# Performance work log

Measured on AMD Instinct MI355X. Metric: run time of the kernel, lower is better.

Reference implementation:

```python
import jax, jax.numpy as jnp
import numpy as np

DIM = 1024
B, SQ, SK = 8, 2048, 2048


def setup_inputs() -> dict:
    key = jax.random.key(0)
    ks = jax.random.split(key, 8)
    s = 1.0 / np.sqrt(DIM)
    return {
        "x": jax.random.normal(ks[0], (B, SQ, DIM), dtype=jnp.float32),
        "context": jax.random.normal(ks[1], (B, SK, DIM), dtype=jnp.float32),
        "Wq": jax.random.normal(ks[2], (DIM, DIM), dtype=jnp.float32) * s,
        "bq": jnp.zeros((DIM,), dtype=jnp.float32),
        "Wk": jax.random.normal(ks[3], (DIM, DIM), dtype=jnp.float32) * s,
        "bk": jnp.zeros((DIM,), dtype=jnp.float32),
        "Wv": jax.random.normal(ks[4], (DIM, DIM), dtype=jnp.float32) * s,
        "bv": jnp.zeros((DIM,), dtype=jnp.float32),
    }


def reference(x, context, Wq, bq, Wk, bk, Wv, bv):
    # nn.Linear: y = x @ W.T + b
    q = jnp.einsum("bsd,ed->bse", x, Wq) + bq          # [B, SQ, D]
    k = jnp.einsum("btd,ed->bte", context, Wk) + bk    # [B, SK, D]
    v = jnp.einsum("btd,ed->bte", context, Wv) + bv    # [B, SK, D]
    scale = 1.0 / jnp.sqrt(jnp.asarray(x.shape[-1], dtype=x.dtype))
    scores = jnp.einsum("bse,bte->bst", q, k) * scale  # [B, SQ, SK]
    attn = jax.nn.softmax(scores, axis=-1)
    return jnp.einsum("bst,bte->bse", attn, v)         # [B, SQ, D]
```

## Files before the change

kernel.cpp:

```cpp
#include <hip/hip_runtime.h>
#include <hip/hip_bf16.h>
#include <hip/hip_fp16.h>

typedef float f32x4 __attribute__((ext_vector_type(4)));
typedef short short8 __attribute__((ext_vector_type(8)));
typedef _Float16 h4 __attribute__((ext_vector_type(4)));
typedef unsigned short u16;
typedef unsigned int u32;

#define LDK 40

__device__ __forceinline__ u16 bf16_rne(float x) {
  u32 u = __float_as_uint(x);
  u += 0x7FFFu + ((u >> 16) & 1u);
  return (u16)(u >> 16);
}
__device__ __forceinline__ u32 pack2(float a, float b) {
  return (u32)bf16_rne(a) | ((u32)bf16_rne(b) << 16);
}

__global__ __launch_bounds__(256)
void convert_kernel(const float* __restrict__ x, const float* __restrict__ ctx,
                    const float* __restrict__ wq, const float* __restrict__ wk,
                    const float* __restrict__ wv,
                    u16* __restrict__ xb, u16* __restrict__ cb,
                    u16* __restrict__ wqb, u16* __restrict__ wkb,
                    u16* __restrict__ wvb)
{
  int blk = blockIdx.x;
  const float* src; u16* dst; size_t off;
  if (blk < 8192)       { src = x;   dst = xb;  off = (size_t)blk * 2048; }
  else if (blk < 16384) { src = ctx; dst = cb;  off = (size_t)(blk - 8192) * 2048; }
  else if (blk < 16896) { src = wq;  dst = wqb; off = (size_t)(blk - 16384) * 2048; }
  else if (blk < 17408) { src = wk;  dst = wkb; off = (size_t)(blk - 16896) * 2048; }
  else                  { src = wv;  dst = wvb; off = (size_t)(blk - 17408) * 2048; }
  size_t e = off + (size_t)threadIdx.x * 8;
  float4 a = *(const float4*)(src + e);
  float4 b = *(const float4*)(src + e + 4);
  uint4 o;
  o.x = pack2(a.x, a.y); o.y = pack2(a.z, a.w);
  o.z = pack2(b.x, b.y); o.w = pack2(b.z, b.w);
  *(uint4*)(dst + e) = o;
}

__device__ __forceinline__ void stage_tile(const u16* __restrict__ G, int ld,
                                           int kt, u16* L, int tid) {
#pragma unroll
  for (int it = 0; it < 2; ++it) {
    int s = tid + 256 * it;
    int r = s >> 2, c = s & 3;
    *(uint4*)&L[r * LDK + c * 8] = *(const uint4*)(G + (size_t)r * ld + kt + c * 8);
  }
}

#define GEMM_FRAGS_AND_MFMA(Ah, Bh)                                            \
  short8 a_f[4], b_f[4];                                                       \
  _Pragma("unroll")                                                            \
  for (int i = 0; i < 4; ++i) {                                                \
    a_f[i] = *(const short8*)&Ah[(wm + i * 16 + lrow) * LDK + quad * 8];       \
    b_f[i] = *(const short8*)&Bh[(wn + i * 16 + lrow) * LDK + quad * 8];       \
  }                                                                            \
  _Pragma("unroll")                                                            \
  for (int i = 0; i < 4; ++i)                                                  \
    _Pragma("unroll")                                                          \
    for (int j = 0; j < 4; ++j)                                                \
      acc[i][j] = __builtin_amdgcn_mfma_f32_16x16x32_bf16(a_f[i], b_f[j], acc[i][j], 0, 0, 0);

#define GEMM_PROLOGUE                                                          \
  const int tid = threadIdx.x;                                                 \
  const int w = tid >> 6, lane = tid & 63;                                     \
  const int wm = (w >> 1) * 64, wn = (w & 1) * 64;                             \
  const int lrow = lane & 15, quad = lane >> 4;                                \
  f32x4 acc[4][4];                                                             \
  _Pragma("unroll")                                                            \
  for (int i = 0; i < 4; ++i)                                                  \
    _Pragma("unroll")                                                          \
    for (int j = 0; j < 4; ++j) {                                              \
      f32x4 z = {0.f, 0.f, 0.f, 0.f};                                          \
      acc[i][j] = z;                                                           \
    }

__global__ __launch_bounds__(256)
void projq_kernel(const u16* __restrict__ A, const u16* __restrict__ W,
                  const float* __restrict__ bias, u16* __restrict__ Y)
{
  __shared__ __align__(16) u16 Ah[128 * LDK];
  __shared__ __align__(16) u16 Bh[128 * LDK];
  const int m0 = blockIdx.y * 128, n0 = blockIdx.x * 128;
  GEMM_PROLOGUE
  const u16* A_b = A + (size_t)m0 * 1024;
  const u16* B_b = W + (size_t)n0 * 1024;

  for (int kt = 0; kt < 1024; kt += 32) {
    __syncthreads();
    stage_tile(A_b, 1024, kt, Ah, tid);
    stage_tile(B_b, 1024, kt, Bh, tid);
    __syncthreads();
    GEMM_FRAGS_AND_MFMA(Ah, Bh)
  }

#pragma unroll
  for (int j = 0; j < 4; ++j) {
    int gn = n0 + wn + j * 16 + lrow;
    float bj = bias[gn];
#pragma unroll
    for (int i = 0; i < 4; ++i) {
      int gm_base = m0 + wm + i * 16 + quad * 4;
#pragma unroll
      for (int r = 0; r < 4; ++r)
        Y[(size_t)(gm_base + r) * 1024 + gn] = bf16_rne(acc[i][j][r] + bj);
    }
  }
}

__global__ __launch_bounds__(256)
void projv_kernel(const u16* __restrict__ A, const u16* __restrict__ W,
                  const float* __restrict__ bias, u16* __restrict__ Vt)
{
  __shared__ __align__(16) u16 smem[128 * 136];
  u16* Ah = smem;
  u16* Bh = smem + 128 * LDK;
  const int m0 = blockIdx.y * 128, n0 = blockIdx.x * 128;
  const int bb = m0 >> 11, t0 = m0 & 2047;
  GEMM_PROLOGUE
  const u16* A_b = A + (size_t)m0 * 1024;
  const u16* B_b = W + (size_t)n0 * 1024;

  for (int kt = 0; kt < 1024; kt += 32) {
    __syncthreads();
    stage_tile(A_b, 1024, kt, Ah, tid);
    stage_tile(B_b, 1024, kt, Bh, tid);
    __syncthreads();
    GEMM_FRAGS_AND_MFMA(Ah, Bh)
  }

  __syncthreads();
  u16* T = smem;
#pragma unroll
  for (int j = 0; j < 4; ++j) {
    int e_l = wn + j * 16 + lrow;
    float bj = bias[n0 + e_l];
#pragma unroll
    for (int i = 0; i < 4; ++i) {
      int t_l = wm + i * 16 + quad * 4;
      uint2 p;
      p.x = pack2(acc[i][j][0] + bj, acc[i][j][1] + bj);
      p.y = pack2(acc[i][j][2] + bj, acc[i][j][3] + bj);
      *(uint2*)&T[e_l * 136 + t_l] = p;
    }
  }
  __syncthreads();

  int e_l = tid >> 1, half = tid & 1;
  u16* gdst = Vt + ((size_t)(bb * 1024 + n0 + e_l)) * 2048 + t0 + half * 64;
  const u16* Trow = &T[e_l * 136 + half * 64];
#pragma unroll
  for (int k = 0; k < 8; ++k)
    *(uint4*)(gdst + k * 8) = *(const uint4*)(Trow + k * 8);
}

__global__ __launch_bounds__(256)
void score_kernel(const u16* __restrict__ qb, const u16* __restrict__ kb,
                  _Float16* __restrict__ S)
{
  __shared__ __align__(16) u16 Ah[128 * LDK];
  __shared__ __align__(16) u16 Bh[128 * LDK];
  const int b = blockIdx.z;
  const int m0 = blockIdx.y * 128, n0 = blockIdx.x * 128;
  GEMM_PROLOGUE
  const u16* A_b = qb + ((size_t)b * 2048 + m0) * 1024;
  const u16* B_b = kb + ((size_t)b * 2048 + n0) * 1024;

  for (int kt = 0; kt < 1024; kt += 32) {
    __syncthreads();
    stage_tile(A_b, 1024, kt, Ah, tid);
    stage_tile(B_b, 1024, kt, Bh, tid);
    __syncthreads();
    GEMM_FRAGS_AND_MFMA(Ah, Bh)
  }

  const float scale = 0.03125f;
#pragma unroll
  for (int j = 0; j < 4; ++j) {
    int gn = n0 + wn + j * 16 + lrow;
#pragma unroll
    for (int i = 0; i < 4; ++i) {
      int gm_base = m0 + wm + i * 16 + quad * 4;
#pragma unroll
      for (int r = 0; r < 4; ++r)
        S[((size_t)b * 2048 + gm_base + r) * 2048 + gn] = (_Float16)(acc[i][j][r] * scale);
    }
  }
}

__global__ __launch_bounds__(256)
void softmax_kernel(_Float16* __restrict__ S)
{
  const int row = blockIdx.x;
  const int tid = threadIdx.x;
  _Float16* Sr = S + (size_t)row * 2048;
  h4 ah = *(const h4*)(Sr + tid * 4);
  h4 bh = *(const h4*)(Sr + 1024 + tid * 4);
  float a0 = (float)ah.x, a1 = (float)ah.y, a2 = (float)ah.z, a3 = (float)ah.w;
  float b0 = (float)bh.x, b1 = (float)bh.y, b2 = (float)bh.z, b3 = (float)bh.w;

  float m = fmaxf(fmaxf(fmaxf(a0, a1), fmaxf(a2, a3)),
                  fmaxf(fmaxf(b0, b1), fmaxf(b2, b3)));
#pragma unroll
  for (int off = 32; off > 0; off >>= 1) m = fmaxf(m, __shfl_xor(m, off));

  __shared__ float red[4];
  const int wid = tid >> 6, lane = tid & 63;
  if (lane == 0) red[wid] = m;
  __syncthreads();
  m = fmaxf(fmaxf(red[0], red[1]), fmaxf(red[2], red[3]));

  float e0 = __expf(a0 - m), e1 = __expf(a1 - m), e2 = __expf(a2 - m), e3 = __expf(a3 - m);
  float e4 = __expf(b0 - m), e5 = __expf(b1 - m), e6 = __expf(b2 - m), e7 = __expf(b3 - m);
  float s = ((e0 + e1) + (e2 + e3)) + ((e4 + e5) + (e6 + e7));
#pragma unroll
  for (int off = 32; off > 0; off >>= 1) s += __shfl_xor(s, off);
  __syncthreads();
  if (lane == 0) red[wid] = s;
  __syncthreads();
  s = red[0] + red[1] + red[2] + red[3];
  float inv = 1.0f / s;

  u16* P = (u16*)S;
  size_t pb = (size_t)row * 2048;
  uint2 w0, w1;
  w0.x = pack2(e0 * inv, e1 * inv);
  w0.y = pack2(e2 * inv, e3 * inv);
  w1.x = pack2(e4 * inv, e5 * inv);
  w1.y = pack2(e6 * inv, e7 * inv);
  *(uint2*)&P[pb + tid * 4] = w0;
  *(uint2*)&P[pb + 1024 + tid * 4] = w1;
}

__global__ __launch_bounds__(256)
void pv_kernel(const u16* __restrict__ P, const u16* __restrict__ Vt,
               float* __restrict__ O)
{
  __shared__ __align__(16) u16 Ah[128 * LDK];
  __shared__ __align__(16) u16 Bh[128 * LDK];
  const int b = blockIdx.z;
  const int m0 = blockIdx.y * 128, n0 = blockIdx.x * 128;
  GEMM_PROLOGUE
  const u16* A_b = P + ((size_t)b * 2048 + m0) * 2048;
  const u16* B_b = Vt + ((size_t)b * 1024 + n0) * 2048;

  for (int kt = 0; kt < 2048; kt += 32) {
    __syncthreads();
    stage_tile(A_b, 2048, kt, Ah, tid);
    stage_tile(B_b, 2048, kt, Bh, tid);
    __syncthreads();
    GEMM_FRAGS_AND_MFMA(Ah, Bh)
  }

#pragma unroll
  for (int j = 0; j < 4; ++j) {
    int gn = n0 + wn + j * 16 + lrow;
#pragma unroll
    for (int i = 0; i < 4; ++i) {
      int gm_base = m0 + wm + i * 16 + quad * 4;
#pragma unroll
      for (int r = 0; r < 4; ++r)
        O[((size_t)b * 2048 + gm_base + r) * 1024 + gn] = acc[i][j][r];
    }
  }
}

extern "C" void kernel_launch(void* const* d_in, const int* in_sizes, int n_in,
                              void* d_out, int out_size, void* d_ws, size_t ws_size,
                              hipStream_t stream) {
  const float* x   = (const float*)d_in[0];
  const float* ctx = (const float*)d_in[1];
  const float* Wq  = (const float*)d_in[2];
  const float* bq  = (const float*)d_in[3];
  const float* Wk  = (const float*)d_in[4];
  const float* bk  = (const float*)d_in[5];
  const float* Wv  = (const float*)d_in[6];
  const float* bv  = (const float*)d_in[7];
  float* out = (float*)d_out;

  const size_t NQ = (size_t)16384 * 1024;
  const size_t NW = (size_t)1024 * 1024;
  const size_t needed = (5 * NQ + 3 * NW) * sizeof(u16);
  if (ws_size < needed) return;

  u16* xb  = (u16*)d_ws;
  u16* cb  = xb + NQ;
  u16* qb  = cb + NQ;
  u16* kb  = qb + NQ;
  u16* vt  = kb + NQ;
  u16* wqb = vt + NQ;
  u16* wkb = wqb + NW;
  u16* wvb = wkb + NW;
  _Float16* S = (_Float16*)d_ws;

  dim3 blk(256, 1, 1);
  hipLaunchKernelGGL(convert_kernel, dim3(17920, 1, 1), blk, 0, stream,
                     x, ctx, Wq, Wk, Wv, xb, cb, wqb, wkb, wvb);
  hipLaunchKernelGGL(projq_kernel, dim3(8, 128, 1), blk, 0, stream, xb, wqb, bq, qb);
  hipLaunchKernelGGL(projq_kernel, dim3(8, 128, 1), blk, 0, stream, cb, wkb, bk, kb);
  hipLaunchKernelGGL(projv_kernel, dim3(8, 128, 1), blk, 0, stream, cb, wvb, bv, vt);
  hipLaunchKernelGGL(score_kernel, dim3(16, 16, 8), blk, 0, stream, qb, kb, S);
  hipLaunchKernelGGL(softmax_kernel, dim3(16384, 1, 1), blk, 0, stream, S);
  hipLaunchKernelGGL(pv_kernel, dim3(8, 16, 8), blk, 0, stream, (const u16*)S, vt, out);
}
```

Before: 595.5 us.

## Stage GEMM tiles via direct global-to-LDS loads with XOR-swizzled layout

Replaces register-staged global→LDS tile copies in all four GEMM kernels with global_load_lds direct-to-LDS transfers. The padded LDK=40 row stride becomes an unpadded 32-wide row with an XOR swizzle on the 16-byte column chunk, applied on both the write and fragment-read sides to avoid bank conflicts. This cuts VGPR traffic and instructions in staging. The loop is still single-buffered with barriers, and correctness depends on the async load being complete at __syncthreads (no explicit vmcnt wait).

```diff
diff --git a/kernel.cpp b/kernel.cpp
--- a/kernel.cpp
+++ b/kernel.cpp
@@ -8,7 +8,7 @@
 typedef unsigned short u16;
 typedef unsigned int u32;
 
-#define LDK 40
+#define BK 32
 
 __device__ __forceinline__ u16 bf16_rne(float x) {
   u32 u = __float_as_uint(x);
@@ -43,13 +43,19 @@
   *(uint4*)(dst + e) = o;
 }
 
-__device__ __forceinline__ void stage_tile(const u16* __restrict__ G, int ld,
-                                           int kt, u16* L, int tid) {
+__device__ __forceinline__ void stage_async(const u16* __restrict__ G, int ld,
+                                            u16* L, int w, int lane)
+{
+  const int r_in = lane >> 2;
+  const int scol = ((lane & 3) ^ ((r_in >> 1) & 3)) * 8;
 #pragma unroll
   for (int it = 0; it < 2; ++it) {
-    int s = tid + 256 * it;
-    int r = s >> 2, c = s & 3;
-    *(uint4*)&L[r * LDK + c * 8] = *(const uint4*)(G + (size_t)r * ld + kt + c * 8);
+    const int rbase = w * 32 + it * 16;
+    const u16* g = G + (size_t)(rbase + r_in) * ld + scol;
+    u16* l = L + rbase * BK;
+    __builtin_amdgcn_global_load_lds(
+        (const __attribute__((address_space(1))) void*)g,
+        (__attribute__((address_space(3))) void*)l, 16, 0, 0);
   }
 }
 
@@ -57,8 +63,8 @@
   short8 a_f[4], b_f[4];                                                       \
   _Pragma("unroll")                                                            \
   for (int i = 0; i < 4; ++i) {                                                \
-    a_f[i] = *(const short8*)&Ah[(wm + i * 16 + lrow) * LDK + quad * 8];       \
-    b_f[i] = *(const short8*)&Bh[(wn + i * 16 + lrow) * LDK + quad * 8];       \
+    a_f[i] = *(const short8*)&Ah[(wm + i * 16 + lrow) * BK + sq8];             \
+    b_f[i] = *(const short8*)&Bh[(wn + i * 16 + lrow) * BK + sq8];             \
   }                                                                            \
   _Pragma("unroll")                                                            \
   for (int i = 0; i < 4; ++i)                                                  \
@@ -71,6 +77,7 @@
   const int w = tid >> 6, lane = tid & 63;                                     \
   const int wm = (w >> 1) * 64, wn = (w & 1) * 64;                             \
   const int lrow = lane & 15, quad = lane >> 4;                                \
+  const int sq8 = (quad ^ ((lrow >> 1) & 3)) * 8;                              \
   f32x4 acc[4][4];                                                             \
   _Pragma("unroll")                                                            \
   for (int i = 0; i < 4; ++i)                                                  \
@@ -84,8 +91,8 @@
 void projq_kernel(const u16* __restrict__ A, const u16* __restrict__ W,
                   const float* __restrict__ bias, u16* __restrict__ Y)
 {
-  __shared__ __align__(16) u16 Ah[128 * LDK];
-  __shared__ __align__(16) u16 Bh[128 * LDK];
+  __shared__ __align__(16) u16 Ah[128 * BK];
+  __shared__ __align__(16) u16 Bh[128 * BK];
   const int m0 = blockIdx.y * 128, n0 = blockIdx.x * 128;
   GEMM_PROLOGUE
   const u16* A_b = A + (size_t)m0 * 1024;
@@ -93,8 +100,8 @@
 
   for (int kt = 0; kt < 1024; kt += 32) {
     __syncthreads();
-    stage_tile(A_b, 1024, kt, Ah, tid);
-    stage_tile(B_b, 1024, kt, Bh, tid);
+    stage_async(A_b + kt, 1024, Ah, w, lane);
+    stage_async(B_b + kt, 1024, Bh, w, lane);
     __syncthreads();
     GEMM_FRAGS_AND_MFMA(Ah, Bh)
   }
@@ -119,7 +126,7 @@
 {
   __shared__ __align__(16) u16 smem[128 * 136];
   u16* Ah = smem;
-  u16* Bh = smem + 128 * LDK;
+  u16* Bh = smem + 128 * BK;
   const int m0 = blockIdx.y * 128, n0 = blockIdx.x * 128;
   const int bb = m0 >> 11, t0 = m0 & 2047;
   GEMM_PROLOGUE
@@ -128,8 +135,8 @@
 
   for (int kt = 0; kt < 1024; kt += 32) {
     __syncthreads();
-    stage_tile(A_b, 1024, kt, Ah, tid);
-    stage_tile(B_b, 1024, kt, Bh, tid);
+    stage_async(A_b + kt, 1024, Ah, w, lane);
+    stage_async(B_b + kt, 1024, Bh, w, lane);
     __syncthreads();
     GEMM_FRAGS_AND_MFMA(Ah, Bh)
   }
@@ -163,8 +170,8 @@
 void score_kernel(const u16* __restrict__ qb, const u16* __restrict__ kb,
                   _Float16* __restrict__ S)
 {
-  __shared__ __align__(16) u16 Ah[128 * LDK];
-  __shared__ __align__(16) u16 Bh[128 * LDK];
+  __shared__ __align__(16) u16 Ah[128 * BK];
+  __shared__ __align__(16) u16 Bh[128 * BK];
   const int b = blockIdx.z;
   const int m0 = blockIdx.y * 128, n0 = blockIdx.x * 128;
   GEMM_PROLOGUE
@@ -173,8 +180,8 @@
 
   for (int kt = 0; kt < 1024; kt += 32) {
     __syncthreads();
-    stage_tile(A_b, 1024, kt, Ah, tid);
-    stage_tile(B_b, 1024, kt, Bh, tid);
+    stage_async(A_b + kt, 1024, Ah, w, lane);
+    stage_async(B_b + kt, 1024, Bh, w, lane);
     __syncthreads();
     GEMM_FRAGS_AND_MFMA(Ah, Bh)
   }
@@ -241,8 +248,8 @@
 void pv_kernel(const u16* __restrict__ P, const u16* __restrict__ Vt,
                float* __restrict__ O)
 {
-  __shared__ __align__(16) u16 Ah[128 * LDK];
-  __shared__ __align__(16) u16 Bh[128 * LDK];
+  __shared__ __align__(16) u16 Ah[128 * BK];
+  __shared__ __align__(16) u16 Bh[128 * BK];
   const int b = blockIdx.z;
   const int m0 = blockIdx.y * 128, n0 = blockIdx.x * 128;
   GEMM_PROLOGUE
@@ -251,8 +258,8 @@
 
   for (int kt = 0; kt < 2048; kt += 32) {
     __syncthreads();
-    stage_tile(A_b, 2048, kt, Ah, tid);
-    stage_tile(B_b, 2048, kt, Bh, tid);
+    stage_async(A_b + kt, 2048, Ah, w, lane);
+    stage_async(B_b + kt, 2048, Bh, w, lane);
     __syncthreads();
     GEMM_FRAGS_AND_MFMA(Ah, Bh)
   }
```

Result: faster. 559.2 us (-6.1%).
